# Kernel tuning notes

Hardware: AMD Instinct MI355X
Metric: run time of the kernel (lower is better)

Reference implementation:

```python
import jax, jax.numpy as jnp
import numpy as np

B = 1024
N = 100  # graph_size
D = 128


def setup_inputs() -> dict:
    key = jax.random.key(0)
    k1, k2 = jax.random.split(key)
    x = jax.random.normal(k1, (B * N, D), dtype=jnp.float32)
    edge_index = jax.random.randint(k2, (2, B * N * (N - 1)), 0, N, dtype=jnp.int64)
    return {"x": x, "edge_index": edge_index, "graph_size": N}


def reference(x, edge_index, graph_size):
    # x: [B*N, D] -> [B, N, D]; edge_index is split but never used in the math.
    b = x.shape[0] // graph_size
    xb = x.reshape(b, graph_size, -1)
    # per-graph dot-product logits: [B, N, N]
    logits = jnp.einsum('bnd,bmd->bnm', xb, xb)
    # segment softmax with index j = column index of the flattened [N*N] logits:
    # normalizes over rows i for each column j -> softmax along axis=1.
    return jax.nn.softmax(logits, axis=1)
```

## Files before the change

kernel.cpp:

```cpp
#include <hip/hip_runtime.h>

#define NG 100
#define DD 128
#define NPAD 112
#define LSTRIDE 136

typedef __attribute__((ext_vector_type(8))) short bf16x8;
typedef __attribute__((ext_vector_type(4))) float floatx4;

__global__ __launch_bounds__(256, 4)
void dotdec_mfma(const float* __restrict__ x, float* __restrict__ out) {
    __shared__ __align__(16) char smraw[NG * NG * 4];
    unsigned short* xs = (unsigned short*)smraw;
    float*          fo = (float*)smraw;

    const int t    = threadIdx.x;
    const int lane = t & 63;
    const int wave = t >> 6;
    const int quad = lane >> 4;
    const int lr   = lane & 15;
    const size_t b = blockIdx.x;
    const float* xb = x   + b * (size_t)(NG * DD);
    float*       ob = out + b * (size_t)(NG * NG);

    if (t < 192) {
        int r = 100 + (t >> 4), c = t & 15;
        *(uint4*)&xs[r * LSTRIDE + c * 8] = make_uint4(0u, 0u, 0u, 0u);
    }
#pragma unroll
    for (int k = 0; k < 7; ++k) {
        int p = t + 256 * k;
        if (p < NG * 16) {
            int n = p >> 4, gp = p & 15;
            float4 v0 = ((const float4*)xb)[n * 32 + gp * 2];
            float4 v1 = ((const float4*)xb)[n * 32 + gp * 2 + 1];
            unsigned int u0 = (__float_as_uint(v0.x) >> 16) | (__float_as_uint(v0.y) & 0xffff0000u);
            unsigned int u1 = (__float_as_uint(v0.z) >> 16) | (__float_as_uint(v0.w) & 0xffff0000u);
            unsigned int u2 = (__float_as_uint(v1.x) >> 16) | (__float_as_uint(v1.y) & 0xffff0000u);
            unsigned int u3 = (__float_as_uint(v1.z) >> 16) | (__float_as_uint(v1.w) & 0xffff0000u);
            *(uint4*)&xs[n * LSTRIDE + gp * 8] = make_uint4(u0, u1, u2, u3);
        }
    }
    __syncthreads();

    const int c0 = wave;
    const int c1 = (wave < 3) ? wave + 4 : wave;
    floatx4 acc[2][7];
#pragma unroll
    for (int ci = 0; ci < 2; ++ci)
#pragma unroll
        for (int t2 = 0; t2 < 7; ++t2) acc[ci][t2] = (floatx4){0.f, 0.f, 0.f, 0.f};

#pragma unroll
    for (int k = 0; k < 4; ++k) {
        const int koff = k * 32 + quad * 8;
        bf16x8 b0 = *(const bf16x8*)&xs[(c0 * 16 + lr) * LSTRIDE + koff];
        bf16x8 b1 = *(const bf16x8*)&xs[(c1 * 16 + lr) * LSTRIDE + koff];
#pragma unroll
        for (int t2 = 0; t2 < 7; ++t2) {
            bf16x8 a = *(const bf16x8*)&xs[(t2 * 16 + lr) * LSTRIDE + koff];
            acc[0][t2] = __builtin_amdgcn_mfma_f32_16x16x32_bf16(a, b0, acc[0][t2], 0, 0, 0);
            acc[1][t2] = __builtin_amdgcn_mfma_f32_16x16x32_bf16(a, b1, acc[1][t2], 0, 0, 0);
        }
    }

    float mx0 = -3.402823466e38f, mx1 = -3.402823466e38f;
#pragma unroll
    for (int t2 = 0; t2 < 6; ++t2)
#pragma unroll
        for (int i = 0; i < 4; ++i) {
            mx0 = fmaxf(mx0, acc[0][t2][i]);
            mx1 = fmaxf(mx1, acc[1][t2][i]);
        }
    if (quad == 0)
#pragma unroll
        for (int i = 0; i < 4; ++i) {
            mx0 = fmaxf(mx0, acc[0][6][i]);
            mx1 = fmaxf(mx1, acc[1][6][i]);
        }
    mx0 = fmaxf(mx0, __shfl_xor(mx0, 16, 64));
    mx0 = fmaxf(mx0, __shfl_xor(mx0, 32, 64));
    mx1 = fmaxf(mx1, __shfl_xor(mx1, 16, 64));
    mx1 = fmaxf(mx1, __shfl_xor(mx1, 32, 64));

    float s0 = 0.f, s1 = 0.f;
#pragma unroll
    for (int t2 = 0; t2 < 6; ++t2)
#pragma unroll
        for (int i = 0; i < 4; ++i) {
            float e0 = __expf(acc[0][t2][i] - mx0); acc[0][t2][i] = e0; s0 += e0;
            float e1 = __expf(acc[1][t2][i] - mx1); acc[1][t2][i] = e1; s1 += e1;
        }
    if (quad == 0)
#pragma unroll
        for (int i = 0; i < 4; ++i) {
            float e0 = __expf(acc[0][6][i] - mx0); acc[0][6][i] = e0; s0 += e0;
            float e1 = __expf(acc[1][6][i] - mx1); acc[1][6][i] = e1; s1 += e1;
        }
    s0 += __shfl_xor(s0, 16, 64); s0 += __shfl_xor(s0, 32, 64);
    s1 += __shfl_xor(s1, 16, 64); s1 += __shfl_xor(s1, 32, 64);
    const float r0 = __builtin_amdgcn_rcpf(s0);
    const float r1 = __builtin_amdgcn_rcpf(s1);

    __syncthreads();
    const int m0 = c0 * 16 + lr;
    const int m1 = c1 * 16 + lr;
    const bool dual = (c1 != c0) && (m1 < NG);
#pragma unroll
    for (int t2 = 0; t2 < 6; ++t2)
#pragma unroll
        for (int i = 0; i < 4; ++i) {
            int n = t2 * 16 + quad * 4 + i;
            fo[n * NG + m0] = acc[0][t2][i] * r0;
            if (dual) fo[n * NG + m1] = acc[1][t2][i] * r1;
        }
    if (quad == 0)
#pragma unroll
        for (int i = 0; i < 4; ++i) {
            int n = 96 + i;
            fo[n * NG + m0] = acc[0][6][i] * r0;
            if (dual) fo[n * NG + m1] = acc[1][6][i] * r1;
        }
    __syncthreads();

#pragma unroll
    for (int k = 0; k < 10; ++k) {
        int f = t + 256 * k;
        if (f < (NG * NG) / 4) {
            float4 v = *(const float4*)&fo[f * 4];
            ((float4*)ob)[f] = v;
        }
    }
}

extern "C" void kernel_launch(void* const* d_in, const int* in_sizes, int n_in,
                              void* d_out, int out_size, void* d_ws, size_t ws_size,
                              hipStream_t stream) {
    const float* x = (const float*)d_in[0];
    float* out = (float*)d_out;
    const int B = in_sizes[0] / (NG * DD);
    hipLaunchKernelGGL(dotdec_mfma, dim3(B), dim3(256), 0, stream, x, out);
}
```

Before: 155.7 us.

## Transpose MFMA operands so softmax columns map to lanes and store outputs directly

```diff
diff --git a/kernel.cpp b/kernel.cpp
--- a/kernel.cpp
+++ b/kernel.cpp
@@ -8,12 +8,24 @@
 typedef __attribute__((ext_vector_type(8))) short bf16x8;
 typedef __attribute__((ext_vector_type(4))) float floatx4;
 
+__device__ __forceinline__ float red_max16(float v) {
+    v = fmaxf(v, __shfl_xor(v, 1, 64));
+    v = fmaxf(v, __shfl_xor(v, 2, 64));
+    v = fmaxf(v, __shfl_xor(v, 4, 64));
+    v = fmaxf(v, __shfl_xor(v, 8, 64));
+    return v;
+}
+__device__ __forceinline__ float red_sum16(float v) {
+    v += __shfl_xor(v, 1, 64);
+    v += __shfl_xor(v, 2, 64);
+    v += __shfl_xor(v, 4, 64);
+    v += __shfl_xor(v, 8, 64);
+    return v;
+}
+
 __global__ __launch_bounds__(256, 4)
 void dotdec_mfma(const float* __restrict__ x, float* __restrict__ out) {
-    __shared__ __align__(16) char smraw[NG * NG * 4];
-    unsigned short* xs = (unsigned short*)smraw;
-    float*          fo = (float*)smraw;
-
+    __shared__ unsigned short xs[NPAD * LSTRIDE];
     const int t    = threadIdx.x;
     const int lane = t & 63;
     const int wave = t >> 6;
@@ -45,90 +57,68 @@
 
     const int c0 = wave;
     const int c1 = (wave < 3) ? wave + 4 : wave;
-    floatx4 acc[2][7];
+    floatx4 acc0[7], acc1[7];
 #pragma unroll
-    for (int ci = 0; ci < 2; ++ci)
-#pragma unroll
-        for (int t2 = 0; t2 < 7; ++t2) acc[ci][t2] = (floatx4){0.f, 0.f, 0.f, 0.f};
-
+    for (int r = 0; r < 7; ++r) {
+        acc0[r] = (floatx4){0.f, 0.f, 0.f, 0.f};
+        acc1[r] = (floatx4){0.f, 0.f, 0.f, 0.f};
+    }
 #pragma unroll
     for (int k = 0; k < 4; ++k) {
         const int koff = k * 32 + quad * 8;
-        bf16x8 b0 = *(const bf16x8*)&xs[(c0 * 16 + lr) * LSTRIDE + koff];
-        bf16x8 b1 = *(const bf16x8*)&xs[(c1 * 16 + lr) * LSTRIDE + koff];
+        bf16x8 a0 = *(const bf16x8*)&xs[(c0 * 16 + lr) * LSTRIDE + koff];
+        bf16x8 a1 = *(const bf16x8*)&xs[(c1 * 16 + lr) * LSTRIDE + koff];
 #pragma unroll
-        for (int t2 = 0; t2 < 7; ++t2) {
-            bf16x8 a = *(const bf16x8*)&xs[(t2 * 16 + lr) * LSTRIDE + koff];
-            acc[0][t2] = __builtin_amdgcn_mfma_f32_16x16x32_bf16(a, b0, acc[0][t2], 0, 0, 0);
-            acc[1][t2] = __builtin_amdgcn_mfma_f32_16x16x32_bf16(a, b1, acc[1][t2], 0, 0, 0);
+        for (int r = 0; r < 7; ++r) {
+            bf16x8 bb = *(const bf16x8*)&xs[(r * 16 + lr) * LSTRIDE + koff];
+            acc0[r] = __builtin_amdgcn_mfma_f32_16x16x32_bf16(a0, bb, acc0[r], 0, 0, 0);
+            acc1[r] = __builtin_amdgcn_mfma_f32_16x16x32_bf16(a1, bb, acc1[r], 0, 0, 0);
         }
     }
 
-    float mx0 = -3.402823466e38f, mx1 = -3.402823466e38f;
+    floatx4 mx0 = acc0[0], mx1 = acc1[0];
 #pragma unroll
-    for (int t2 = 0; t2 < 6; ++t2)
+    for (int r = 1; r < 7; ++r)
 #pragma unroll
-        for (int i = 0; i < 4; ++i) {
-            mx0 = fmaxf(mx0, acc[0][t2][i]);
-            mx1 = fmaxf(mx1, acc[1][t2][i]);
+        for (int j = 0; j < 4; ++j) {
+            mx0[j] = fmaxf(mx0[j], acc0[r][j]);
+            mx1[j] = fmaxf(mx1[j], acc1[r][j]);
         }
-    if (quad == 0)
 #pragma unroll
-        for (int i = 0; i < 4; ++i) {
-            mx0 = fmaxf(mx0, acc[0][6][i]);
-            mx1 = fmaxf(mx1, acc[1][6][i]);
+    for (int j = 0; j < 4; ++j) {
+        mx0[j] = red_max16(mx0[j]);
+        mx1[j] = red_max16(mx1[j]);
+    }
+
+    floatx4 s0 = (floatx4){0.f, 0.f, 0.f, 0.f};
+    floatx4 s1 = (floatx4){0.f, 0.f, 0.f, 0.f};
+#pragma unroll
+    for (int r = 0; r < 7; ++r)
+#pragma unroll
+        for (int j = 0; j < 4; ++j) {
+            float e0 = __expf(acc0[r][j] - mx0[j]); acc0[r][j] = e0; s0[j] += e0;
+            float e1 = __expf(acc1[r][j] - mx1[j]); acc1[r][j] = e1; s1[j] += e1;
         }
-    mx0 = fmaxf(mx0, __shfl_xor(mx0, 16, 64));
-    mx0 = fmaxf(mx0, __shfl_xor(mx0, 32, 64));
-    mx1 = fmaxf(mx1, __shfl_xor(mx1, 16, 64));
-    mx1 = fmaxf(mx1, __shfl_xor(mx1, 32, 64));
+    floatx4 inv0, inv1;
+#pragma unroll
+    for (int j = 0; j < 4; ++j) {
+        inv0[j] = __builtin_amdgcn_rcpf(red_sum16(s0[j]));
+        inv1[j] = __builtin_amdgcn_rcpf(red_sum16(s1[j]));
+    }
 
-    float s0 = 0.f, s1 = 0.f;
+    const bool dual = (wave < 3) && !(c1 == 6 && quad != 0);
+    const int mo0 = c0 * 16 + quad * 4;
+    const int mo1 = c1 * 16 + quad * 4;
 #pragma unroll
-    for (int t2 = 0; t2 < 6; ++t2)
-#pragma unroll
-        for (int i = 0; i < 4; ++i) {
-            float e0 = __expf(acc[0][t2][i] - mx0); acc[0][t2][i] = e0; s0 += e0;
-            float e1 = __expf(acc[1][t2][i] - mx1); acc[1][t2][i] = e1; s1 += e1;
-        }
-    if (quad == 0)
-#pragma unroll
-        for (int i = 0; i < 4; ++i) {
-            float e0 = __expf(acc[0][6][i] - mx0); acc[0][6][i] = e0; s0 += e0;
-            float e1 = __expf(acc[1][6][i] - mx1); acc[1][6][i] = e1; s1 += e1;
-        }
-    s0 += __shfl_xor(s0, 16, 64); s0 += __shfl_xor(s0, 32, 64);
-    s1 += __shfl_xor(s1, 16, 64); s1 += __shfl_xor(s1, 32, 64);
-    const float r0 = __builtin_amdgcn_rcpf(s0);
-    const float r1 = __builtin_amdgcn_rcpf(s1);
-
-    __syncthreads();
-    const int m0 = c0 * 16 + lr;
-    const int m1 = c1 * 16 + lr;
-    const bool dual = (c1 != c0) && (m1 < NG);
-#pragma unroll
-    for (int t2 = 0; t2 < 6; ++t2)
-#pragma unroll
-        for (int i = 0; i < 4; ++i) {
-            int n = t2 * 16 + quad * 4 + i;
-            fo[n * NG + m0] = acc[0][t2][i] * r0;
-            if (dual) fo[n * NG + m1] = acc[1][t2][i] * r1;
-        }
-    if (quad == 0)
-#pragma unroll
-        for (int i = 0; i < 4; ++i) {
-            int n = 96 + i;
-            fo[n * NG + m0] = acc[0][6][i] * r0;
-            if (dual) fo[n * NG + m1] = acc[1][6][i] * r1;
-        }
-    __syncthreads();
-
-#pragma unroll
-    for (int k = 0; k < 10; ++k) {
-        int f = t + 256 * k;
-        if (f < (NG * NG) / 4) {
-            float4 v = *(const float4*)&fo[f * 4];
-            ((float4*)ob)[f] = v;
+    for (int r = 0; r < 7; ++r) {
+        int n = r * 16 + lr;
+        if (n < NG) {
+            floatx4 o0 = acc0[r] * inv0;
+            *(floatx4*)&ob[n * NG + mo0] = o0;
+            if (dual) {
+                floatx4 o1 = acc1[r] * inv1;
+                *(floatx4*)&ob[n * NG + mo1] = o1;
+            }
         }
     }
 }
```

Result: slower. 160.0 us (+2.7%).
